# Performance work log

Measured on AMD Instinct MI355X. Metric: run time of the kernel, lower is better.

Reference implementation:

```python
import jax, jax.numpy as jnp
import numpy as np

ATOM_TYPES = (1, 6, 7, 8)  # H, C, N, O
BN_EPS = 1e-3


def setup_inputs() -> dict:
    key = jax.random.key(0)
    k1, k2, k3 = jax.random.split(key, 3)
    B, N, M, d, L = 16, 2048, 64, 3, 12
    X = jax.random.normal(k1, (B, N, d), jnp.float32) * 4.0  # coords in Angstrom-ish scale
    # neighbor indices; offset trick guarantees no self-neighbor (avoids R=0)
    off = jax.random.randint(k2, (B, N, M), 1, N)
    Nbrs = ((jnp.arange(N)[None, :, None] + off) % N).astype(jnp.int32)
    Nbrs_Z = jax.random.randint(k3, (B, N, M), 0, 10).astype(jnp.int32)
    params = np.array([[rc, rs, 4.0] for rc in (4.0, 8.0) for rs in (0.0, 1.0, 2.0, 3.0, 4.0, 5.0)], np.float32)
    rc = jnp.asarray(params[:, 0].reshape(L, 1, 1, 1))
    rs = jnp.asarray(params[:, 1].reshape(L, 1, 1, 1))
    re = jnp.asarray(params[:, 2].reshape(L, 1, 1, 1))
    return {"X": X, "Nbrs": Nbrs, "Nbrs_Z": Nbrs_Z, "rc": rc, "rs": rs, "re": re}


def reference(X, Nbrs, Nbrs_Z, rc, rs, re):
    # gather neighbor coordinates: [B,N,M,d]
    nbr = jax.vmap(lambda coords, idx: coords[idx])(X, Nbrs)
    D = nbr - X[:, :, None, :]                      # displacement tensor [B,N,M,d]
    R = jnp.sqrt(jnp.sum(D * D, axis=-1))           # distance matrix  [B,N,M]
    R1 = R[None]                                    # [1,B,N,M], broadcasts vs [L,1,1,1]
    K = jnp.exp(-re * (R1 - rs) ** 2)               # gaussian        [L,B,N,M]
    FC = jnp.where(R1 <= rc, 0.5 * (jnp.cos(jnp.pi * R1 / rc) + 1.0), 0.0)
    rsf = K * FC                                    # radial symmetry fn [L,B,N,M]
    # per-atom-type masks [A,B,N,M]
    types = jnp.asarray(ATOM_TYPES, Nbrs_Z.dtype)
    conds = (Nbrs_Z[None] == types[:, None, None, None]).astype(rsf.dtype)
    # masked reduce over neighbors, concat over types (type-major) -> [A*L,B,N]
    sym = jnp.einsum('abnm,lbnm->albn', conds, rsf)
    A, L = sym.shape[0], sym.shape[1]
    layer = sym.reshape(A * L, sym.shape[2], sym.shape[3]).transpose(1, 2, 0)  # [B,N,A*L]
    # tf.nn.moments over axis 0 (biased variance) + batch_normalization (no scale/offset)
    m = jnp.mean(layer, axis=0)
    v = jnp.var(layer, axis=0)
    return (layer - m) / jnp.sqrt(v + BN_EPS)
```

## Files before the change

kernel.cpp:

```cpp
#include <hip/hip_runtime.h>

#define NB 16
#define NN 2048
#define NM 64
#define NC 48
#define LDSP 49
#define PIF 3.14159265358979323f

struct F3 { float x, y, z; };

__device__ __forceinline__ float rfl(float v) {
  return __uint_as_float(__builtin_amdgcn_readfirstlane(__float_as_uint(v)));
}

__global__ __launch_bounds__(256, 8) void fused_kernel(
    const float* __restrict__ X,
    const int* __restrict__ Nbrs,
    const int* __restrict__ NbrsZ,
    const float* __restrict__ rcg,
    const float* __restrict__ rsg,
    const float* __restrict__ reg,
    float* __restrict__ out)
{
  __shared__ float sBN[NB * LDSP];

  const int tid = threadIdx.x;
  const int b   = tid >> 4;
  const int t   = tid & 15;
  const int s   = t & 7;
  const int h   = t >> 3;
  const int n   = blockIdx.x;
  const int row = b * NN + n;

  const float rc4 = rcg[0], rc8 = rcg[6];
  const float re  = reg[0];
  const float nre = -re;
  const float pio8  = rfl(PIF / rc8);
  const float sp    = rsg[1] - rsg[0];
  const float gcoef = rfl(2.f * re * sp);
  const float rs3   = rsg[3];
  const float qu4 = rfl(__expf(nre * (rsg[4] * rsg[4] - rsg[3] * rsg[3])));
  const float qu5 = rfl(__expf(nre * (rsg[5] * rsg[5] - rsg[4] * rsg[4])));
  const float qd2 = rfl(__expf(nre * (rsg[2] * rsg[2] - rsg[3] * rsg[3])));
  const float qd1 = rfl(__expf(nre * (rsg[1] * rsg[1] - rsg[2] * rsg[2])));
  const float qd0 = rfl(__expf(nre * (rsg[0] * rsg[0] - rsg[1] * rsg[1])));

  const float* xb = X + (size_t)b * (NN * 3);
  const float xi = xb[n * 3 + 0];
  const float yi = xb[n * 3 + 1];
  const float zi = xb[n * 3 + 2];

  float2 acc2[12];
#pragma unroll
  for (int q = 0; q < 12; ++q) acc2[q] = make_float2(0.f, 0.f);

#pragma unroll
  for (int chunk = 0; chunk < 2; ++chunk) {
    const int base = row * NM + s * 8 + chunk * 4;
    const int4 j4 = *(const int4*)(Nbrs  + base);
    const int4 z4 = *(const int4*)(NbrsZ + base);
    const int js[4] = {j4.x, j4.y, j4.z, j4.w};
    const int zs[4] = {z4.x, z4.y, z4.z, z4.w};

    float R[4];
#pragma unroll
    for (int u = 0; u < 4; ++u) {
      const F3 p = *(const F3*)(xb + js[u] * 3);
      const float dx = p.x - xi, dy = p.y - yi, dz = p.z - zi;
      R[u] = sqrtf(fmaf(dx, dx, fmaf(dy, dy, dz * dz)));
    }

#pragma unroll
    for (int u = 0; u < 4; ++u) {
      const float Rv = R[u];
      const float Rk = fminf(Rv, rc8);

      const float u3 = Rk - rs3;
      const float K3 = __expf(nre * (u3 * u3));
      const float Gu = __expf(gcoef * Rk);
      const float Gd = __builtin_amdgcn_rcpf(Gu);
      const float K4 = K3 * Gu * qu4;
      const float K5 = K4 * Gu * qu5;
      const float K2 = K3 * Gd * qd2;
      const float K1 = K2 * Gd * qd1;
      const float K0 = K1 * Gd * qd0;
      const float K[6] = {K0, K1, K2, K3, K4, K5};

      const float c8  = __cosf(pio8 * Rv);
      const float c4  = fmaf(c8 + c8, c8, -1.f);
      const float fc8 = (Rv <= rc8) ? fmaf(0.5f, c8, 0.5f) : 0.f;
      const float fc4 = (Rv <= rc4) ? fmaf(0.5f, c4, 0.5f) : 0.f;
      const float fcX = h ? fc8 : fc4;

      const int z = zs[u];
      const float a0 = (z == 1) ? fcX : 0.f;
      const float a1 = (z == 6) ? fcX : 0.f;
      const float a2 = (z == 7) ? fcX : 0.f;
      const float a3 = (z == 8) ? fcX : 0.f;

#pragma unroll
      for (int p = 0; p < 3; ++p) {
        const float k0 = K[2 * p], k1 = K[2 * p + 1];
        acc2[0 + p].x = fmaf(a0, k0, acc2[0 + p].x);
        acc2[0 + p].y = fmaf(a0, k1, acc2[0 + p].y);
        acc2[3 + p].x = fmaf(a1, k0, acc2[3 + p].x);
        acc2[3 + p].y = fmaf(a1, k1, acc2[3 + p].y);
        acc2[6 + p].x = fmaf(a2, k0, acc2[6 + p].x);
        acc2[6 + p].y = fmaf(a2, k1, acc2[6 + p].y);
        acc2[9 + p].x = fmaf(a3, k0, acc2[9 + p].x);
        acc2[9 + p].y = fmaf(a3, k1, acc2[9 + p].y);
      }
    }
  }

  float acc[24];
#pragma unroll
  for (int q = 0; q < 12; ++q) {
    acc[2 * q]     = acc2[q].x;
    acc[2 * q + 1] = acc2[q].y;
  }

#pragma unroll
  for (int c = 0; c < 24; ++c) acc[c] += __shfl_xor(acc[c], 4, 64);
  const bool s4 = (s & 4) != 0;
#pragma unroll
  for (int j = 0; j < 12; ++j) acc[j] = s4 ? acc[12 + j] : acc[j];
#pragma unroll
  for (int j = 0; j < 12; ++j) acc[j] += __shfl_xor(acc[j], 2, 64);
  const bool s2 = (s & 2) != 0;
#pragma unroll
  for (int j = 0; j < 6; ++j) acc[j] = s2 ? acc[6 + j] : acc[j];
#pragma unroll
  for (int j = 0; j < 6; ++j) acc[j] += __shfl_xor(acc[j], 1, 64);
  const bool s1 = (s & 1) != 0;
#pragma unroll
  for (int j = 0; j < 3; ++j) acc[j] = s1 ? acc[3 + j] : acc[j];

  const int gb = b * LDSP + (s >> 1) * 12 + h * 6 + 3 * (s & 1);
  sBN[gb + 0] = acc[0];
  sBN[gb + 1] = acc[1];
  sBN[gb + 2] = acc[2];

  __syncthreads();

  if (tid < NC) {
    const int cc = tid;
    float x[NB];
    float sm = 0.f;
#pragma unroll
    for (int bb = 0; bb < NB; ++bb) {
      x[bb] = sBN[bb * LDSP + cc];
      sm += x[bb];
    }
    const float mean = sm * (1.f / NB);
    float vs = 0.f;
#pragma unroll
    for (int bb = 0; bb < NB; ++bb) {
      const float d = x[bb] - mean;
      vs = fmaf(d, d, vs);
    }
    const float inv = rsqrtf(vs * (1.f / NB) + 1e-3f);
#pragma unroll
    for (int bb = 0; bb < NB; ++bb) {
      out[(size_t)bb * (NN * NC) + n * NC + cc] = (x[bb] - mean) * inv;
    }
  }
}

extern "C" void kernel_launch(void* const* d_in, const int* in_sizes, int n_in,
                              void* d_out, int out_size, void* d_ws, size_t ws_size,
                              hipStream_t stream) {
  const float* X   = (const float*)d_in[0];
  const int* Nbrs  = (const int*)d_in[1];
  const int* NbrsZ = (const int*)d_in[2];
  const float* rcg = (const float*)d_in[3];
  const float* rsg = (const float*)d_in[4];
  const float* reg = (const float*)d_in[5];

  float* out = (float*)d_out;

  fused_kernel<<<2048, 256, 0, stream>>>(X, Nbrs, NbrsZ, rcg, rsg, reg, out);
}
```

Measured before the change: 20.86 us.

## Spread each row's neighbors over a full wavefront with 1024-thread blocks

Each block now uses 1024 threads, one 64-lane wavefront per batch, and each lane handles 2 neighbors instead of 8. This raises thread-level parallelism and shortens the per-thread serial chain of gathers and transcendentals. In exchange the butterfly reduction gains an extra shuffle stage, the per-thread constant setup is repeated across four times as many threads, and __launch_bounds__(1024, 8) may tighten register limits.

```diff
diff --git a/kernel.cpp b/kernel.cpp
--- a/kernel.cpp
+++ b/kernel.cpp
@@ -13,7 +13,7 @@
   return __uint_as_float(__builtin_amdgcn_readfirstlane(__float_as_uint(v)));
 }
 
-__global__ __launch_bounds__(256, 8) void fused_kernel(
+__global__ __launch_bounds__(1024, 8) void fused_kernel(
     const float* __restrict__ X,
     const int* __restrict__ Nbrs,
     const int* __restrict__ NbrsZ,
@@ -25,10 +25,10 @@
   __shared__ float sBN[NB * LDSP];
 
   const int tid = threadIdx.x;
-  const int b   = tid >> 4;
-  const int t   = tid & 15;
-  const int s   = t & 7;
-  const int h   = t >> 3;
+  const int b   = tid >> 6;
+  const int t   = tid & 63;
+  const int h   = t >> 5;
+  const int s   = t & 31;
   const int n   = blockIdx.x;
   const int row = b * NN + n;
 
@@ -50,66 +50,63 @@
   const float yi = xb[n * 3 + 1];
   const float zi = xb[n * 3 + 2];
 
+  const int base = row * NM + 2 * s;
+  const int2 j2 = *(const int2*)(Nbrs  + base);
+  const int2 z2 = *(const int2*)(NbrsZ + base);
+  const int js[2] = {j2.x, j2.y};
+  const int zs[2] = {z2.x, z2.y};
+
+  float R[2];
+#pragma unroll
+  for (int u = 0; u < 2; ++u) {
+    const F3 p = *(const F3*)(xb + js[u] * 3);
+    const float dx = p.x - xi, dy = p.y - yi, dz = p.z - zi;
+    R[u] = sqrtf(fmaf(dx, dx, fmaf(dy, dy, dz * dz)));
+  }
+
   float2 acc2[12];
 #pragma unroll
   for (int q = 0; q < 12; ++q) acc2[q] = make_float2(0.f, 0.f);
 
 #pragma unroll
-  for (int chunk = 0; chunk < 2; ++chunk) {
-    const int base = row * NM + s * 8 + chunk * 4;
-    const int4 j4 = *(const int4*)(Nbrs  + base);
-    const int4 z4 = *(const int4*)(NbrsZ + base);
-    const int js[4] = {j4.x, j4.y, j4.z, j4.w};
-    const int zs[4] = {z4.x, z4.y, z4.z, z4.w};
+  for (int u = 0; u < 2; ++u) {
+    const float Rv = R[u];
+    const float Rk = fminf(Rv, rc8);
 
-    float R[4];
-#pragma unroll
-    for (int u = 0; u < 4; ++u) {
-      const F3 p = *(const F3*)(xb + js[u] * 3);
-      const float dx = p.x - xi, dy = p.y - yi, dz = p.z - zi;
-      R[u] = sqrtf(fmaf(dx, dx, fmaf(dy, dy, dz * dz)));
-    }
+    const float u3 = Rk - rs3;
+    const float K3 = __expf(nre * (u3 * u3));
+    const float Gu = __expf(gcoef * Rk);
+    const float Gd = __builtin_amdgcn_rcpf(Gu);
+    const float K4 = K3 * Gu * qu4;
+    const float K5 = K4 * Gu * qu5;
+    const float K2 = K3 * Gd * qd2;
+    const float K1 = K2 * Gd * qd1;
+    const float K0 = K1 * Gd * qd0;
+    const float K[6] = {K0, K1, K2, K3, K4, K5};
+
+    const float c8  = __cosf(pio8 * Rv);
+    const float c4  = fmaf(c8 + c8, c8, -1.f);
+    const float fc8 = (Rv <= rc8) ? fmaf(0.5f, c8, 0.5f) : 0.f;
+    const float fc4 = (Rv <= rc4) ? fmaf(0.5f, c4, 0.5f) : 0.f;
+    const float fcX = h ? fc8 : fc4;
+
+    const int z = zs[u];
+    const float a0 = (z == 1) ? fcX : 0.f;
+    const float a1 = (z == 6) ? fcX : 0.f;
+    const float a2 = (z == 7) ? fcX : 0.f;
+    const float a3 = (z == 8) ? fcX : 0.f;
 
 #pragma unroll
-    for (int u = 0; u < 4; ++u) {
-      const float Rv = R[u];
-      const float Rk = fminf(Rv, rc8);
-
-      const float u3 = Rk - rs3;
-      const float K3 = __expf(nre * (u3 * u3));
-      const float Gu = __expf(gcoef * Rk);
-      const float Gd = __builtin_amdgcn_rcpf(Gu);
-      const float K4 = K3 * Gu * qu4;
-      const float K5 = K4 * Gu * qu5;
-      const float K2 = K3 * Gd * qd2;
-      const float K1 = K2 * Gd * qd1;
-      const float K0 = K1 * Gd * qd0;
-      const float K[6] = {K0, K1, K2, K3, K4, K5};
-
-      const float c8  = __cosf(pio8 * Rv);
-      const float c4  = fmaf(c8 + c8, c8, -1.f);
-      const float fc8 = (Rv <= rc8) ? fmaf(0.5f, c8, 0.5f) : 0.f;
-      const float fc4 = (Rv <= rc4) ? fmaf(0.5f, c4, 0.5f) : 0.f;
-      const float fcX = h ? fc8 : fc4;
-
-      const int z = zs[u];
-      const float a0 = (z == 1) ? fcX : 0.f;
-      const float a1 = (z == 6) ? fcX : 0.f;
-      const float a2 = (z == 7) ? fcX : 0.f;
-      const float a3 = (z == 8) ? fcX : 0.f;
-
-#pragma unroll
-      for (int p = 0; p < 3; ++p) {
-        const float k0 = K[2 * p], k1 = K[2 * p + 1];
-        acc2[0 + p].x = fmaf(a0, k0, acc2[0 + p].x);
-        acc2[0 + p].y = fmaf(a0, k1, acc2[0 + p].y);
-        acc2[3 + p].x = fmaf(a1, k0, acc2[3 + p].x);
-        acc2[3 + p].y = fmaf(a1, k1, acc2[3 + p].y);
-        acc2[6 + p].x = fmaf(a2, k0, acc2[6 + p].x);
-        acc2[6 + p].y = fmaf(a2, k1, acc2[6 + p].y);
-        acc2[9 + p].x = fmaf(a3, k0, acc2[9 + p].x);
-        acc2[9 + p].y = fmaf(a3, k1, acc2[9 + p].y);
-      }
+    for (int p = 0; p < 3; ++p) {
+      const float k0 = K[2 * p], k1 = K[2 * p + 1];
+      acc2[0 + p].x = fmaf(a0, k0, acc2[0 + p].x);
+      acc2[0 + p].y = fmaf(a0, k1, acc2[0 + p].y);
+      acc2[3 + p].x = fmaf(a1, k0, acc2[3 + p].x);
+      acc2[3 + p].y = fmaf(a1, k1, acc2[3 + p].y);
+      acc2[6 + p].x = fmaf(a2, k0, acc2[6 + p].x);
+      acc2[6 + p].y = fmaf(a2, k1, acc2[6 + p].y);
+      acc2[9 + p].x = fmaf(a3, k0, acc2[9 + p].x);
+      acc2[9 + p].y = fmaf(a3, k1, acc2[9 + p].y);
     }
   }
 
@@ -121,25 +118,35 @@
   }
 
 #pragma unroll
-  for (int c = 0; c < 24; ++c) acc[c] += __shfl_xor(acc[c], 4, 64);
-  const bool s4 = (s & 4) != 0;
+  for (int c = 0; c < 24; ++c) acc[c] += __shfl_xor(acc[c], 16, 64);
+  const bool k16 = (s & 16) != 0;
 #pragma unroll
-  for (int j = 0; j < 12; ++j) acc[j] = s4 ? acc[12 + j] : acc[j];
+  for (int j = 0; j < 12; ++j) acc[j] = k16 ? acc[12 + j] : acc[j];
 #pragma unroll
-  for (int j = 0; j < 12; ++j) acc[j] += __shfl_xor(acc[j], 2, 64);
-  const bool s2 = (s & 2) != 0;
+  for (int j = 0; j < 12; ++j) acc[j] += __shfl_xor(acc[j], 8, 64);
+  const bool k8 = (s & 8) != 0;
 #pragma unroll
-  for (int j = 0; j < 6; ++j) acc[j] = s2 ? acc[6 + j] : acc[j];
+  for (int j = 0; j < 6; ++j) acc[j] = k8 ? acc[6 + j] : acc[j];
 #pragma unroll
-  for (int j = 0; j < 6; ++j) acc[j] += __shfl_xor(acc[j], 1, 64);
-  const bool s1 = (s & 1) != 0;
+  for (int j = 0; j < 6; ++j) acc[j] += __shfl_xor(acc[j], 4, 64);
+  const bool k4 = (s & 4) != 0;
 #pragma unroll
-  for (int j = 0; j < 3; ++j) acc[j] = s1 ? acc[3 + j] : acc[j];
+  for (int j = 0; j < 3; ++j) acc[j] = k4 ? acc[3 + j] : acc[j];
+#pragma unroll
+  for (int j = 0; j < 3; ++j) acc[j] += __shfl_xor(acc[j], 2, 64);
+  const bool k2 = (s & 2) != 0;
+  acc[0] = k2 ? acc[2] : acc[0];
+  acc[0] += __shfl_xor(acc[0], 1, 64);
+  acc[1] += __shfl_xor(acc[1], 1, 64);
+  const int q = s & 3;
 
-  const int gb = b * LDSP + (s >> 1) * 12 + h * 6 + 3 * (s & 1);
-  sBN[gb + 0] = acc[0];
-  sBN[gb + 1] = acc[1];
-  sBN[gb + 2] = acc[2];
+  if (q != 3) {
+    const float val = (q == 1) ? acc[1] : acc[0];
+    const int c  = 12 * ((s >> 4) & 1) + 6 * ((s >> 3) & 1) + 3 * ((s >> 2) & 1) + q;
+    const int ty = c / 6;
+    const int r  = c - ty * 6;
+    sBN[b * LDSP + ty * 12 + h * 6 + r] = val;
+  }
 
   __syncthreads();
 
@@ -179,5 +186,5 @@
 
   float* out = (float*)d_out;
 
-  fused_kernel<<<2048, 256, 0, stream>>>(X, Nbrs, NbrsZ, rcg, rsg, reg, out);
+  fused_kernel<<<2048, 1024, 0, stream>>>(X, Nbrs, NbrsZ, rcg, rsg, reg, out);
 }
```

After: 24.87 us. +19.2%, slower.
